# Performance work log

Measured on AMD Instinct MI355X. Metric: run time of the kernel, lower is better.

## Reference

```python
import jax, jax.numpy as jnp
import numpy as np

D_MODEL = 1024
NUM_HEADS = 16
NUM_KV_HEADS = 4
D_K = D_MODEL // NUM_HEADS          # 64
GROUP = NUM_HEADS // NUM_KV_HEADS   # 4
D_KV = D_MODEL // GROUP             # 256


def setup_inputs() -> dict:
    key = jax.random.key(0)
    ks = jax.random.split(key, 12)
    B, S = 2, 2048
    sc = 0.02
    return {
        "query": jax.random.normal(ks[0], (B, S, D_MODEL), jnp.float32),
        "key": jax.random.normal(ks[1], (B, S, D_MODEL), jnp.float32),
        "value": jax.random.normal(ks[2], (B, S, D_MODEL), jnp.float32),
        "w_q": jax.random.normal(ks[3], (D_MODEL, D_MODEL), jnp.float32) * sc,
        "b_q": jnp.zeros((D_MODEL,), jnp.float32),
        "w_k": jax.random.normal(ks[4], (D_KV, D_MODEL), jnp.float32) * sc,
        "b_k": jnp.zeros((D_KV,), jnp.float32),
        "w_v": jax.random.normal(ks[5], (D_KV, D_MODEL), jnp.float32) * sc,
        "b_v": jnp.zeros((D_KV,), jnp.float32),
        "w_o": jax.random.normal(ks[6], (D_MODEL, D_MODEL), jnp.float32) * sc,
        "b_o": jnp.zeros((D_MODEL,), jnp.float32),
    }


def reference(query, key, value, w_q, b_q, w_k, b_k, w_v, b_v, w_o, b_o):
    B, S, _ = query.shape
    # projections (torch Linear: x @ W.T + b)
    Q = query @ w_q.T + b_q            # [B,S,d_model]
    K = key @ w_k.T + b_k              # [B,S,d_kv]
    V = value @ w_v.T + b_v            # [B,S,d_kv]
    # [B, Hkv, G, S, Dk] for Q; [B, Hkv, S, Dk] for K/V.
    # repeat_interleave(group, dim=1) on K/V == sharing each KV head across
    # its group of query heads, so we contract without duplicating K/V.
    Q = Q.reshape(B, S, NUM_KV_HEADS, GROUP, D_K).transpose(0, 2, 3, 1, 4)
    K = K.reshape(B, S, NUM_KV_HEADS, D_K).transpose(0, 2, 1, 3)
    V = V.reshape(B, S, NUM_KV_HEADS, D_K).transpose(0, 2, 1, 3)
    scale = 1.0 / jnp.sqrt(jnp.asarray(D_K, Q.dtype))
    scores = jnp.einsum('bhgsd,bhtd->bhgst', Q, K) * scale  # [B,Hkv,G,S,S]
    attn = jax.nn.softmax(scores, axis=-1)
    out = jnp.einsum('bhgst,bhtd->bhgsd', attn, V)          # [B,Hkv,G,S,Dk]
    # -> [B,S,Hkv*G*Dk] = [B,S,d_model]
    out = out.transpose(0, 3, 1, 2, 4).reshape(B, S, D_MODEL)
    return out @ w_o.T + b_o
```

## Files before the change

kernel.cpp:

```cpp
#include <hip/hip_runtime.h>
#include <hip/hip_bf16.h>
#include <stdint.h>

typedef unsigned short u16;
typedef unsigned int   u32;
typedef short s16x8 __attribute__((ext_vector_type(8)));
typedef u16   u16x4 __attribute__((ext_vector_type(4)));
typedef u16   u16x8 __attribute__((ext_vector_type(8)));
typedef float f32x4  __attribute__((ext_vector_type(4)));
typedef float f32x16 __attribute__((ext_vector_type(16)));
typedef float f4     __attribute__((ext_vector_type(4)));
typedef u32   u32x4  __attribute__((ext_vector_type(4)));

#define MFMA(a,b,c)   __builtin_amdgcn_mfma_f32_16x16x32_bf16((a),(b),(c),0,0,0)
#define MFMA32(a,b,c) __builtin_amdgcn_mfma_f32_32x32x16_bf16((a),(b),(c),0,0,0)

__device__ __forceinline__ u16 f2b(float f){
  union { float f; unsigned u; } v; v.f = f;
  unsigned r = v.u + 0x7fffu + ((v.u >> 16) & 1u);
  return (u16)(r >> 16);
}

__device__ __forceinline__ u32 cvtpk(float lo, float hi){
  u32 r;
  asm("v_cvt_pk_bf16_f32 %0, %1, %2" : "=v"(r) : "v"(lo), "v"(hi));
  return r;
}

__device__ __forceinline__ float exp2h(float x){
  float r;
  asm("v_exp_f32 %0, %1" : "=v"(r) : "v"(x));
  return r;
}

__device__ __forceinline__ void gll16(const void* g, void* l){
  __builtin_amdgcn_global_load_lds(
      (const __attribute__((address_space(1))) void*)g,
      (__attribute__((address_space(3))) void*)l, 16, 0, 0);
}

__global__ __launch_bounds__(256) void wcast(const float* __restrict__ wq,
                                             const float* __restrict__ wk,
                                             const float* __restrict__ wv,
                                             const float* __restrict__ wo,
                                             u16* dq, u16* dk, u16* dv, u16* dov){
  int e = (blockIdx.x * 256 + threadIdx.x) * 4;
  const float* s; u16* d; int off;
  if      (e < 1048576){ s = wq; d = dq;  off = 0; }
  else if (e < 1310720){ s = wk; d = dk;  off = 1048576; }
  else if (e < 1572864){ s = wv; d = dv;  off = 1310720; }
  else                 { s = wo; d = dov; off = 1572864; }
  int i = e - off;
  f4 v = *(const f4*)(s + i);
  u16x4 o;
  o[0] = f2b(v[0]); o[1] = f2b(v[1]); o[2] = f2b(v[2]); o[3] = f2b(v[3]);
  *(u16x4*)(d + i) = o;
}

__global__ __launch_bounds__(256) void qkv_gemm(
    const float* __restrict__ qa, const float* __restrict__ ka, const float* __restrict__ va,
    const u16* __restrict__ wq, const u16* __restrict__ wk, const u16* __restrict__ wv,
    const float* __restrict__ bq, const float* __restrict__ bk, const float* __restrict__ bv,
    u16* Qo, u16* Ko, u16* Vo){
  __shared__ u16 As[2][128*32];
  __shared__ u16 Bs[2][128*32];
  const int tid = threadIdx.x, lane = tid & 63, wid = tid >> 6;
  const int bid = blockIdx.x;
  const float* A; const u16* B; const float* bias; u16* C; int N; float cscale; int bm, bn;
  if (bid < 256)      { A=qa; B=wq; bias=bq; C=Qo; N=1024; cscale=0.18033688011112f; bm=bid>>3;       bn=bid&7; }
  else if (bid < 320) { A=ka; B=wk; bias=bk; C=Ko; N=256;  cscale=1.0f;              bm=(bid-256)>>1; bn=(bid-256)&1; }
  else                { A=va; B=wv; bias=bv; C=Vo; N=256;  cscale=1.0f;              bm=(bid-320)>>1; bn=(bid-320)&1; }
  const int wr = wid >> 1, wc = wid & 1;
  const int r15 = lane & 15, kg = lane >> 4;

  const u16*  Bg = B + (size_t)bn * 128 * 1024;
  const float* Ag = A + (size_t)bm * 128 * 1024;
  f32x4 acc[4][4] = {};

  #pragma unroll
  for (int i = 0; i < 2; i++){
    int cc = wid + i*4, row = cc*16 + (lane >> 2);
    gll16((const char*)Bg + ((size_t)row*1024)*2 + (lane & 3)*16, (char*)&Bs[0][0] + cc*1024);
  }
  #pragma unroll
  for (int p = 0; p < 4; p++){
    int c = tid + p*256, row = c >> 3, c4 = (c & 7) << 2;
    f4 v = *(const f4*)(Ag + (size_t)row*1024 + c4);
    u16x4 o; o[0]=f2b(v[0]); o[1]=f2b(v[1]); o[2]=f2b(v[2]); o[3]=f2b(v[3]);
    *(u16x4*)&As[0][row*32 + c4] = o;
  }
  __syncthreads();

  for (int k0 = 0; k0 < 1024; k0 += 32){
    const int cur = (k0 >> 5) & 1;
    const bool pf = (k0 + 32) < 1024;
    f4 areg[4];
    if (pf){
      #pragma unroll
      for (int i = 0; i < 2; i++){
        int cc = wid + i*4, row = cc*16 + (lane >> 2);
        gll16((const char*)Bg + ((size_t)row*1024 + k0 + 32)*2 + (lane & 3)*16,
              (char*)&Bs[cur^1][0] + cc*1024);
      }
      #pragma unroll
      for (int p = 0; p < 4; p++){
        int c = tid + p*256, row = c >> 3, c4 = (c & 7) << 2;
        areg[p] = *(const f4*)(Ag + (size_t)row*1024 + k0 + 32 + c4);
      }
    }
    s16x8 af[4], bf[4];
    #pragma unroll
    for (int i = 0; i < 4; i++)
      af[i] = *(const s16x8*)&As[cur][(wr*64 + i*16 + r15)*32 + kg*8];
    #pragma unroll
    for (int j = 0; j < 4; j++)
      bf[j] = *(const s16x8*)&Bs[cur][(wc*64 + j*16 + r15)*32 + kg*8];
    __builtin_amdgcn_s_setprio(1);
    #pragma unroll
    for (int i = 0; i < 4; i++)
      #pragma unroll
      for (int j = 0; j < 4; j++)
        acc[i][j] = MFMA(af[i], bf[j], acc[i][j]);
    __builtin_amdgcn_s_setprio(0);
    if (pf){
      #pragma unroll
      for (int p = 0; p < 4; p++){
        int c = tid + p*256, row = c >> 3, c4 = (c & 7) << 2;
        u16x4 o; o[0]=f2b(areg[p][0]); o[1]=f2b(areg[p][1]); o[2]=f2b(areg[p][2]); o[3]=f2b(areg[p][3]);
        *(u16x4*)&As[cur^1][row*32 + c4] = o;
      }
    }
    __syncthreads();
  }
  #pragma unroll
  for (int i = 0; i < 4; i++){
    int row = bm*128 + wr*64 + i*16 + kg*4;
    #pragma unroll
    for (int j = 0; j < 4; j++){
      int col = bn*128 + wc*64 + j*16 + r15;
      float bj = bias[col];
      #pragma unroll
      for (int r = 0; r < 4; r++)
        C[(size_t)(row + r)*N + col] = f2b((acc[i][j][r] + bj) * cscale);
    }
  }
}

__global__ __launch_bounds__(256) void gemm_o(const u16* __restrict__ Aw,
                                              const u16* __restrict__ Bw,
                                              const float* __restrict__ bias,
                                              float* __restrict__ Cv){
  __shared__ u16 As[2][128*32];
  __shared__ u16 Bs[2][128*32];
  const int tid = threadIdx.x, lane = tid & 63, wid = tid >> 6;
  const int bm = blockIdx.x >> 3, bn = blockIdx.x & 7;
  const int wr = wid >> 1, wc = wid & 1;
  const int r15 = lane & 15, kg = lane >> 4;
  const u16* Ag = Aw + (size_t)bm * 128 * 1024;
  const u16* Bg = Bw + (size_t)bn * 128 * 1024;
  f32x4 acc[4][4] = {};

  auto stage = [&](int buf, int k0){
    #pragma unroll
    for (int i = 0; i < 2; i++){
      int cc = wid + i*4, row = cc*16 + (lane >> 2);
      gll16((const char*)Ag + ((size_t)row*1024 + k0)*2 + (lane & 3)*16, (char*)&As[buf][0] + cc*1024);
      gll16((const char*)Bg + ((size_t)row*1024 + k0)*2 + (lane & 3)*16, (char*)&Bs[buf][0] + cc*1024);
    }
  };
  stage(0, 0);
  __syncthreads();
  for (int k0 = 0; k0 < 1024; k0 += 32){
    const int cur = (k0 >> 5) & 1;
    if (k0 + 32 < 1024) stage(cur ^ 1, k0 + 32);
    s16x8 af[4], bf[4];
    #pragma unroll
    for (int i = 0; i < 4; i++)
      af[i] = *(const s16x8*)&As[cur][(wr*64 + i*16 + r15)*32 + kg*8];
    #pragma unroll
    for (int j = 0; j < 4; j++)
      bf[j] = *(const s16x8*)&Bs[cur][(wc*64 + j*16 + r15)*32 + kg*8];
    __builtin_amdgcn_s_setprio(1);
    #pragma unroll
    for (int i = 0; i < 4; i++)
      #pragma unroll
      for (int j = 0; j < 4; j++)
        acc[i][j] = MFMA(af[i], bf[j], acc[i][j]);
    __builtin_amdgcn_s_setprio(0);
    __syncthreads();
  }
  #pragma unroll
  for (int i = 0; i < 4; i++){
    int row = bm*128 + wr*64 + i*16 + kg*4;
    #pragma unroll
    for (int j = 0; j < 4; j++){
      int col = bn*128 + wc*64 + j*16 + r15;
      float bj = bias[col];
      #pragma unroll
      for (int r = 0; r < 4; r++)
        Cv[(size_t)(row + r)*1024 + col] = acc[i][j][r] + bj;
    }
  }
}

__global__ __launch_bounds__(256) void transpose_v(const u16* __restrict__ V,
                                                   u16* __restrict__ Vt){
  __shared__ u16 tile[64][72];
  const int bx = blockIdx.x;
  const int tt = bx & 31, kvh = (bx >> 5) & 3, b = bx >> 7;
  const int tid = threadIdx.x;
  #pragma unroll
  for (int p = 0; p < 2; p++){
    int c = tid + p*256;
    int t = c >> 3, d8 = (c & 7) * 8;
    u16x8 v = *(const u16x8*)(V + (size_t)(b*2048 + tt*64 + t)*256 + kvh*64 + d8);
    *(u16x8*)&tile[t][d8] = v;
  }
  __syncthreads();
  #pragma unroll
  for (int p = 0; p < 2; p++){
    int c = tid + p*256;
    int dd = c >> 3, t8 = (c & 7) * 8;
    u16x8 o;
    #pragma unroll
    for (int j = 0; j < 8; j++) o[j] = tile[t8 + j][dd];
    *(u16x8*)(Vt + ((size_t)((b*4 + kvh)*64 + dd) * 2048 + tt*64 + t8)) = o;
  }
}

__global__ __launch_bounds__(256, 2) void attn_fwd(const u16* __restrict__ Qp,
                                                   const u16* __restrict__ Kp,
                                                   const u16* __restrict__ Vt,
                                                   u16* __restrict__ Op){
  __shared__ u16 Ks[2][64*64];
  __shared__ u16 Vs[2][64*64];
  const int tid = threadIdx.x, lane = tid & 63, w = tid >> 6;
  const int bx = blockIdx.x;
  const int qt = bx & 15, h = (bx >> 4) & 15, b = bx >> 8;
  const int kvh = h >> 2;
  const int l31 = lane & 31, hh = lane >> 5;
  const int srow = lane >> 3;
  const int scol16 = ((lane & 7) ^ srow) << 4;

  const size_t qrow0 = (size_t)(b*2048 + qt*128 + w*32 + l31) << 10;
  s16x8 qf[4];
  #pragma unroll
  for (int db = 0; db < 4; db++)
    qf[db] = *(const s16x8*)(Qp + qrow0 + h*64 + db*16 + hh*8);

  f32x16 oacc[2] = {};
  const f32x16 ZERO = {};
  float lsum = 0.f;

  auto stage = [&](int buf, int t0){
    #pragma unroll
    for (int i = 0; i < 2; i++){
      int cc = w + i*4;
      int row = cc*8 + srow;
      const u16* ksrc = Kp + ((size_t)(b*2048 + t0 + row) << 8) + kvh*64;
      gll16((const char*)ksrc + scol16, (char*)&Ks[buf][0] + cc*1024);
      const u16* vsrc = Vt + ((size_t)((b*4 + kvh)*64 + row) << 11) + t0;
      gll16((const char*)vsrc + scol16, (char*)&Vs[buf][0] + cc*1024);
    }
  };

  stage(0, 0);
  __syncthreads();

  for (int t0 = 0; t0 < 2048; t0 += 64){
    const int cur = (t0 >> 6) & 1;
    if (t0 + 64 < 2048) stage(cur ^ 1, t0 + 64);

    f32x16 sacc[2];
    __builtin_amdgcn_s_setprio(1);
    #pragma unroll
    for (int kb2 = 0; kb2 < 2; kb2++){
      #pragma unroll
      for (int db = 0; db < 4; db++){
        int row = kb2*32 + l31;
        int slot = (db*2 + hh) ^ (row & 7);
        s16x8 kf = *(const s16x8*)((const char*)&Ks[cur][0] + row*128 + slot*16);
        sacc[kb2] = MFMA32(kf, qf[db], (db == 0) ? ZERO : sacc[kb2]);
      }
    }
    __builtin_amdgcn_s_setprio(0);

    u32 W[2][4][2];
    #pragma unroll
    for (int kb2 = 0; kb2 < 2; kb2++){
      float p[16];
      #pragma unroll
      for (int r = 0; r < 16; r++){
        p[r] = exp2h(sacc[kb2][r]);
        lsum += p[r];
      }
      #pragma unroll
      for (int a = 0; a < 4; a++){
        W[kb2][a][0] = cvtpk(p[4*a + 0], p[4*a + 1]);
        W[kb2][a][1] = cvtpk(p[4*a + 2], p[4*a + 3]);
      }
    }

    s16x8 pa[4];
    #pragma unroll
    for (int kq = 0; kq < 4; kq++){
      const int kb2 = kq >> 1, c = kq & 1;
      u32 t[2];
      #pragma unroll
      for (int pp = 0; pp < 2; pp++){
        u32 x = hh ? W[kb2][2*c][pp] : W[kb2][2*c + 1][pp];
        t[pp] = (u32)__shfl_xor((int)x, 32, 64);
      }
      u32x4 dw;
      dw[0] = hh ? t[0] : W[kb2][2*c][0];
      dw[1] = hh ? t[1] : W[kb2][2*c][1];
      dw[2] = hh ? W[kb2][2*c + 1][0] : t[0];
      dw[3] = hh ? W[kb2][2*c + 1][1] : t[1];
      pa[kq] = *(const s16x8*)&dw;
    }

    __builtin_amdgcn_s_setprio(1);
    #pragma unroll
    for (int dblk = 0; dblk < 2; dblk++){
      #pragma unroll
      for (int kq = 0; kq < 4; kq++){
        int row = dblk*32 + l31;
        int slot = (kq*2 + hh) ^ (row & 7);
        s16x8 vf = *(const s16x8*)((const char*)&Vs[cur][0] + row*128 + slot*16);
        oacc[dblk] = MFMA32(pa[kq], vf, oacc[dblk]);
      }
    }
    __builtin_amdgcn_s_setprio(0);
    __syncthreads();
  }

  float rsum = lsum + __shfl_xor(lsum, 32, 64);
  float rinv = __builtin_amdgcn_rcpf(rsum);
  const size_t obase = (size_t)(b*2048 + qt*128 + w*32) << 10;
  #pragma unroll
  for (int reg = 0; reg < 16; reg++){
    const int qrow = (reg & 3) + 4*hh + 8*(reg >> 2);
    float rq = __shfl(rinv, qrow, 64);
    #pragma unroll
    for (int dblk = 0; dblk < 2; dblk++){
      float v = oacc[dblk][reg] * rq;
      Op[obase + ((size_t)qrow << 10) + h*64 + dblk*32 + l31] = f2b(v);
    }
  }
}

extern "C" void kernel_launch(void* const* d_in, const int* in_sizes, int n_in,
                              void* d_out, int out_size, void* d_ws, size_t ws_size,
                              hipStream_t stream){
  const float* query = (const float*)d_in[0];
  const float* key   = (const float*)d_in[1];
  const float* value = (const float*)d_in[2];
  const float* w_q   = (const float*)d_in[3];
  const float* b_q   = (const float*)d_in[4];
  const float* w_k   = (const float*)d_in[5];
  const float* b_k   = (const float*)d_in[6];
  const float* w_v   = (const float*)d_in[7];
  const float* b_v   = (const float*)d_in[8];
  const float* w_o   = (const float*)d_in[9];
  const float* b_o   = (const float*)d_in[10];

  char* ws = (char*)d_ws;
  size_t off = 0;
  u16* wqb = (u16*)(ws + off); off += (size_t)1024*1024*2;
  u16* wkb = (u16*)(ws + off); off += (size_t)256*1024*2;
  u16* wvb = (u16*)(ws + off); off += (size_t)256*1024*2;
  u16* wob = (u16*)(ws + off); off += (size_t)1024*1024*2;
  u16* Qw  = (u16*)(ws + off); off += (size_t)4096*1024*2;
  u16* Kw  = (u16*)(ws + off); off += (size_t)4096*256*2;
  u16* Vw  = (u16*)(ws + off); off += (size_t)4096*256*2;
  u16* Vtw = (u16*)(ws + off); off += (size_t)4096*256*2;
  u16* AOw = (u16*)(ws + off); off += (size_t)4096*1024*2;

  wcast<<<2560, 256, 0, stream>>>(w_q, w_k, w_v, w_o, wqb, wkb, wvb, wob);

  qkv_gemm<<<384, 256, 0, stream>>>(query, key, value, wqb, wkb, wvb,
                                    b_q, b_k, b_v, Qw, Kw, Vw);

  transpose_v<<<256, 256, 0, stream>>>(Vw, Vtw);
  attn_fwd<<<512, 256, 0, stream>>>(Qw, Kw, Vtw, AOw);

  gemm_o<<<256, 256, 0, stream>>>(AOw, wob, b_o, (float*)d_out);
}
```

Before: 120.1 us.

## Fuse V transpose into QKV GEMM, split attention KV range across two wave groups

The V projection epilogue now writes V directly in transposed layout, so the separate transpose kernel and its extra buffer are gone. The attention kernel doubles its block to 512 threads, and two wave groups each process alternating halves of the key range. Their partial outputs and row sums are merged through shared memory at the end. Bf16 packing now uses v_cvt_pk_bf16_f32, and the lane exchange uses v_permlane32_swap in place of shuffles. In exchange, shared memory use doubles, the final merge adds a block-wide sync, and the transposed V stores are strided.

After: 110.3 us. -8.1%, faster.

```diff
diff --git a/kernel.cpp b/kernel.cpp
--- a/kernel.cpp
+++ b/kernel.cpp
@@ -7,10 +7,11 @@
 typedef short s16x8 __attribute__((ext_vector_type(8)));
 typedef u16   u16x4 __attribute__((ext_vector_type(4)));
 typedef u16   u16x8 __attribute__((ext_vector_type(8)));
+typedef u32   u32x2 __attribute__((ext_vector_type(2)));
+typedef u32   u32x4 __attribute__((ext_vector_type(4)));
 typedef float f32x4  __attribute__((ext_vector_type(4)));
 typedef float f32x16 __attribute__((ext_vector_type(16)));
 typedef float f4     __attribute__((ext_vector_type(4)));
-typedef u32   u32x4  __attribute__((ext_vector_type(4)));
 
 #define MFMA(a,b,c)   __builtin_amdgcn_mfma_f32_16x16x32_bf16((a),(b),(c),0,0,0)
 #define MFMA32(a,b,c) __builtin_amdgcn_mfma_f32_32x32x16_bf16((a),(b),(c),0,0,0)
@@ -52,24 +53,24 @@
   else                 { s = wo; d = dov; off = 1572864; }
   int i = e - off;
   f4 v = *(const f4*)(s + i);
-  u16x4 o;
-  o[0] = f2b(v[0]); o[1] = f2b(v[1]); o[2] = f2b(v[2]); o[3] = f2b(v[3]);
-  *(u16x4*)(d + i) = o;
+  u32x2 o; o[0] = cvtpk(v[0], v[1]); o[1] = cvtpk(v[2], v[3]);
+  *(u32x2*)(d + i) = o;
 }
 
 __global__ __launch_bounds__(256) void qkv_gemm(
     const float* __restrict__ qa, const float* __restrict__ ka, const float* __restrict__ va,
     const u16* __restrict__ wq, const u16* __restrict__ wk, const u16* __restrict__ wv,
     const float* __restrict__ bq, const float* __restrict__ bk, const float* __restrict__ bv,
-    u16* Qo, u16* Ko, u16* Vo){
+    u16* Qo, u16* Ko, u16* Vto){
   __shared__ u16 As[2][128*32];
   __shared__ u16 Bs[2][128*32];
   const int tid = threadIdx.x, lane = tid & 63, wid = tid >> 6;
   const int bid = blockIdx.x;
-  const float* A; const u16* B; const float* bias; u16* C; int N; float cscale; int bm, bn;
-  if (bid < 256)      { A=qa; B=wq; bias=bq; C=Qo; N=1024; cscale=0.18033688011112f; bm=bid>>3;       bn=bid&7; }
-  else if (bid < 320) { A=ka; B=wk; bias=bk; C=Ko; N=256;  cscale=1.0f;              bm=(bid-256)>>1; bn=(bid-256)&1; }
-  else                { A=va; B=wv; bias=bv; C=Vo; N=256;  cscale=1.0f;              bm=(bid-320)>>1; bn=(bid-320)&1; }
+  const float* A; const u16* B; const float* bias; int N; float cscale; int bm, bn;
+  bool isV = false;
+  if (bid < 256)      { A=qa; B=wq; bias=bq; N=1024; cscale=0.18033688011112f; bm=bid>>3;       bn=bid&7; }
+  else if (bid < 320) { A=ka; B=wk; bias=bk; N=256;  cscale=1.0f;              bm=(bid-256)>>1; bn=(bid-256)&1; }
+  else                { A=va; B=wv; bias=bv; N=256;  cscale=1.0f;              bm=(bid-320)>>1; bn=(bid-320)&1; isV = true; }
   const int wr = wid >> 1, wc = wid & 1;
   const int r15 = lane & 15, kg = lane >> 4;
 
@@ -86,8 +87,8 @@
   for (int p = 0; p < 4; p++){
     int c = tid + p*256, row = c >> 3, c4 = (c & 7) << 2;
     f4 v = *(const f4*)(Ag + (size_t)row*1024 + c4);
-    u16x4 o; o[0]=f2b(v[0]); o[1]=f2b(v[1]); o[2]=f2b(v[2]); o[3]=f2b(v[3]);
-    *(u16x4*)&As[0][row*32 + c4] = o;
+    u32x2 o; o[0] = cvtpk(v[0], v[1]); o[1] = cvtpk(v[2], v[3]);
+    *(u32x2*)&As[0][row*32 + c4] = o;
   }
   __syncthreads();
 
@@ -126,22 +127,41 @@
       #pragma unroll
       for (int p = 0; p < 4; p++){
         int c = tid + p*256, row = c >> 3, c4 = (c & 7) << 2;
-        u16x4 o; o[0]=f2b(areg[p][0]); o[1]=f2b(areg[p][1]); o[2]=f2b(areg[p][2]); o[3]=f2b(areg[p][3]);
-        *(u16x4*)&As[cur^1][row*32 + c4] = o;
+        u32x2 o; o[0] = cvtpk(areg[p][0], areg[p][1]); o[1] = cvtpk(areg[p][2], areg[p][3]);
+        *(u32x2*)&As[cur^1][row*32 + c4] = o;
       }
     }
     __syncthreads();
   }
-  #pragma unroll
-  for (int i = 0; i < 4; i++){
-    int row = bm*128 + wr*64 + i*16 + kg*4;
-    #pragma unroll
-    for (int j = 0; j < 4; j++){
-      int col = bn*128 + wc*64 + j*16 + r15;
-      float bj = bias[col];
-      #pragma unroll
-      for (int r = 0; r < 4; r++)
-        C[(size_t)(row + r)*N + col] = f2b((acc[i][j][r] + bj) * cscale);
+
+  if (isV){
+    #pragma unroll
+    for (int i = 0; i < 4; i++){
+      int row0 = bm*128 + wr*64 + i*16 + kg*4;
+      int bb = row0 >> 11, t = row0 & 2047;
+      #pragma unroll
+      for (int j = 0; j < 4; j++){
+        int col = bn*128 + wc*64 + j*16 + r15;
+        float bj = bias[col];
+        u16x4 vv;
+        #pragma unroll
+        for (int r = 0; r < 4; r++) vv[r] = f2b(acc[i][j][r] + bj);
+        *(u16x4*)&Vto[((size_t)(bb*256 + col) << 11) + t] = vv;
+      }
+    }
+  } else {
+    u16* C = (bid < 256) ? Qo : Ko;
+    #pragma unroll
+    for (int i = 0; i < 4; i++){
+      int row = bm*128 + wr*64 + i*16 + kg*4;
+      #pragma unroll
+      for (int j = 0; j < 4; j++){
+        int col = bn*128 + wc*64 + j*16 + r15;
+        float bj = bias[col];
+        #pragma unroll
+        for (int r = 0; r < 4; r++)
+          C[(size_t)(row + r)*N + col] = f2b((acc[i][j][r] + bj) * cscale);
+      }
     }
   }
 }
@@ -203,38 +223,14 @@
   }
 }
 
-__global__ __launch_bounds__(256) void transpose_v(const u16* __restrict__ V,
-                                                   u16* __restrict__ Vt){
-  __shared__ u16 tile[64][72];
-  const int bx = blockIdx.x;
-  const int tt = bx & 31, kvh = (bx >> 5) & 3, b = bx >> 7;
-  const int tid = threadIdx.x;
-  #pragma unroll
-  for (int p = 0; p < 2; p++){
-    int c = tid + p*256;
-    int t = c >> 3, d8 = (c & 7) * 8;
-    u16x8 v = *(const u16x8*)(V + (size_t)(b*2048 + tt*64 + t)*256 + kvh*64 + d8);
-    *(u16x8*)&tile[t][d8] = v;
-  }
-  __syncthreads();
-  #pragma unroll
-  for (int p = 0; p < 2; p++){
-    int c = tid + p*256;
-    int dd = c >> 3, t8 = (c & 7) * 8;
-    u16x8 o;
-    #pragma unroll
-    for (int j = 0; j < 8; j++) o[j] = tile[t8 + j][dd];
-    *(u16x8*)(Vt + ((size_t)((b*4 + kvh)*64 + dd) * 2048 + tt*64 + t8)) = o;
-  }
-}
-
-__global__ __launch_bounds__(256, 2) void attn_fwd(const u16* __restrict__ Qp,
+__global__ __launch_bounds__(512, 4) void attn_fwd(const u16* __restrict__ Qp,
                                                    const u16* __restrict__ Kp,
                                                    const u16* __restrict__ Vt,
                                                    u16* __restrict__ Op){
-  __shared__ u16 Ks[2][64*64];
-  __shared__ u16 Vs[2][64*64];
+  __shared__ u16 Ks[2][2][64*64];
+  __shared__ u16 Vs[2][2][64*64];
   const int tid = threadIdx.x, lane = tid & 63, w = tid >> 6;
+  const int wg = w & 3, g = w >> 2;
   const int bx = blockIdx.x;
   const int qt = bx & 15, h = (bx >> 4) & 15, b = bx >> 8;
   const int kvh = h >> 2;
@@ -242,7 +238,7 @@
   const int srow = lane >> 3;
   const int scol16 = ((lane & 7) ^ srow) << 4;
 
-  const size_t qrow0 = (size_t)(b*2048 + qt*128 + w*32 + l31) << 10;
+  const size_t qrow0 = (size_t)(b*2048 + qt*128 + wg*32 + l31) << 10;
   s16x8 qf[4];
   #pragma unroll
   for (int db = 0; db < 4; db++)
@@ -255,21 +251,21 @@
   auto stage = [&](int buf, int t0){
     #pragma unroll
     for (int i = 0; i < 2; i++){
-      int cc = w + i*4;
+      int cc = wg + i*4;
       int row = cc*8 + srow;
       const u16* ksrc = Kp + ((size_t)(b*2048 + t0 + row) << 8) + kvh*64;
-      gll16((const char*)ksrc + scol16, (char*)&Ks[buf][0] + cc*1024);
+      gll16((const char*)ksrc + scol16, (char*)&Ks[g][buf][0] + cc*1024);
       const u16* vsrc = Vt + ((size_t)((b*4 + kvh)*64 + row) << 11) + t0;
-      gll16((const char*)vsrc + scol16, (char*)&Vs[buf][0] + cc*1024);
+      gll16((const char*)vsrc + scol16, (char*)&Vs[g][buf][0] + cc*1024);
     }
   };
 
-  stage(0, 0);
+  stage(0, g*64);
   __syncthreads();
 
-  for (int t0 = 0; t0 < 2048; t0 += 64){
-    const int cur = (t0 >> 6) & 1;
-    if (t0 + 64 < 2048) stage(cur ^ 1, t0 + 64);
+  for (int it = 0; it < 16; it++){
+    const int cur = it & 1;
+    if (it + 1 < 16) stage(cur ^ 1, (2*(it + 1) + g)*64);
 
     f32x16 sacc[2];
     __builtin_amdgcn_s_setprio(1);
@@ -279,7 +275,7 @@
       for (int db = 0; db < 4; db++){
         int row = kb2*32 + l31;
         int slot = (db*2 + hh) ^ (row & 7);
-        s16x8 kf = *(const s16x8*)((const char*)&Ks[cur][0] + row*128 + slot*16);
+        s16x8 kf = *(const s16x8*)((const char*)&Ks[g][cur][0] + row*128 + slot*16);
         sacc[kb2] = MFMA32(kf, qf[db], (db == 0) ? ZERO : sacc[kb2]);
       }
     }
@@ -305,17 +301,13 @@
     #pragma unroll
     for (int kq = 0; kq < 4; kq++){
       const int kb2 = kq >> 1, c = kq & 1;
-      u32 t[2];
+      u32x4 dw;
       #pragma unroll
       for (int pp = 0; pp < 2; pp++){
-        u32 x = hh ? W[kb2][2*c][pp] : W[kb2][2*c + 1][pp];
-        t[pp] = (u32)__shfl_xor((int)x, 32, 64);
-      }
-      u32x4 dw;
-      dw[0] = hh ? t[0] : W[kb2][2*c][0];
-      dw[1] = hh ? t[1] : W[kb2][2*c][1];
-      dw[2] = hh ? W[kb2][2*c + 1][0] : t[0];
-      dw[3] = hh ? W[kb2][2*c + 1][1] : t[1];
+        u32 x = W[kb2][2*c][pp], y = W[kb2][2*c + 1][pp];
+        asm volatile("v_permlane32_swap_b32 %0, %1" : "+v"(x), "+v"(y));
+        dw[pp] = x; dw[2 + pp] = y;
+      }
       pa[kq] = *(const s16x8*)&dw;
     }
 
@@ -326,7 +318,7 @@
       for (int kq = 0; kq < 4; kq++){
         int row = dblk*32 + l31;
         int slot = (kq*2 + hh) ^ (row & 7);
-        s16x8 vf = *(const s16x8*)((const char*)&Vs[cur][0] + row*128 + slot*16);
+        s16x8 vf = *(const s16x8*)((const char*)&Vs[g][cur][0] + row*128 + slot*16);
         oacc[dblk] = MFMA32(pa[kq], vf, oacc[dblk]);
       }
     }
@@ -335,16 +327,32 @@
   }
 
   float rsum = lsum + __shfl_xor(lsum, 32, 64);
-  float rinv = __builtin_amdgcn_rcpf(rsum);
-  const size_t obase = (size_t)(b*2048 + qt*128 + w*32) << 10;
-  #pragma unroll
-  for (int reg = 0; reg < 16; reg++){
-    const int qrow = (reg & 3) + 4*hh + 8*(reg >> 2);
-    float rq = __shfl(rinv, qrow, 64);
-    #pragma unroll
-    for (int dblk = 0; dblk < 2; dblk++){
-      float v = oacc[dblk][reg] * rq;
-      Op[obase + ((size_t)qrow << 10) + h*64 + dblk*32 + l31] = f2b(v);
+  float* Om = (float*)&Ks[0][0][0];
+  float* Ls = (float*)&Vs[0][0][0];
+  if (g == 1){
+    #pragma unroll
+    for (int reg = 0; reg < 16; reg++){
+      int q = (reg & 3) + 4*hh + 8*(reg >> 2);
+      #pragma unroll
+      for (int dblk = 0; dblk < 2; dblk++)
+        Om[(wg*32 + q)*64 + dblk*32 + l31] = oacc[dblk][reg];
+    }
+    if (hh == 0) Ls[wg*32 + l31] = rsum;
+  }
+  __syncthreads();
+  if (g == 0){
+    rsum += Ls[wg*32 + l31];
+    float rinv = __builtin_amdgcn_rcpf(rsum);
+    const size_t obase = (size_t)(b*2048 + qt*128 + wg*32) << 10;
+    #pragma unroll
+    for (int reg = 0; reg < 16; reg++){
+      const int qrow = (reg & 3) + 4*hh + 8*(reg >> 2);
+      float rq = __shfl(rinv, qrow, 64);
+      #pragma unroll
+      for (int dblk = 0; dblk < 2; dblk++){
+        float v = (oacc[dblk][reg] + Om[(wg*32 + qrow)*64 + dblk*32 + l31]) * rq;
+        Op[obase + ((size_t)qrow << 10) + h*64 + dblk*32 + l31] = f2b(v);
+      }
     }
   }
 }
@@ -372,17 +380,15 @@
   u16* wob = (u16*)(ws + off); off += (size_t)1024*1024*2;
   u16* Qw  = (u16*)(ws + off); off += (size_t)4096*1024*2;
   u16* Kw  = (u16*)(ws + off); off += (size_t)4096*256*2;
-  u16* Vw  = (u16*)(ws + off); off += (size_t)4096*256*2;
   u16* Vtw = (u16*)(ws + off); off += (size_t)4096*256*2;
   u16* AOw = (u16*)(ws + off); off += (size_t)4096*1024*2;
 
   wcast<<<2560, 256, 0, stream>>>(w_q, w_k, w_v, w_o, wqb, wkb, wvb, wob);
 
   qkv_gemm<<<384, 256, 0, stream>>>(query, key, value, wqb, wkb, wvb,
-                                    b_q, b_k, b_v, Qw, Kw, Vw);
-
-  transpose_v<<<256, 256, 0, stream>>>(Vw, Vtw);
-  attn_fwd<<<512, 256, 0, stream>>>(Qw, Kw, Vtw, AOw);
+                                    b_q, b_k, b_v, Qw, Kw, Vtw);
+
+  attn_fwd<<<512, 512, 0, stream>>>(Qw, Kw, Vtw, AOw);
 
   gemm_o<<<256, 256, 0, stream>>>(AOw, wob, b_o, (float*)d_out);
 }
```
